# Kernel optimization log

Measured on AMD Instinct MI355X. Metric: run time of the kernel, lower is better.

The kernel has to match this reference:

```python
import jax, jax.numpy as jnp
import numpy as np

SEQ_LEN, PRED_LEN = 512, 96
D_MODEL, D_STATE, D_FF = 512, 16, 512
DT_RANK = 32  # ceil(d_model / 16)
E_LAYERS = 2
B, N = 32, 256


def _layernorm(x, g, b, eps=1e-5):
    mu = jnp.mean(x, -1, keepdims=True)
    var = jnp.mean((x - mu) ** 2, -1, keepdims=True)
    return (x - mu) * jax.lax.rsqrt(var + eps) * g + b


def _mamba(x, win, convw, convb, wx, wdt, bdt, alog, dparam, wout):
    # x: [B, T, D] with T = n_variates + 6 (inverted tokens)
    Bb, T, D = x.shape
    xz = x @ win.T                      # [B, T, 2D] (expand=1 -> d_inner = D)
    xr, z = xz[..., :D], xz[..., D:]
    # causal depthwise conv, d_conv=2: y[t] = w0*x[t-1] + w1*x[t] + b
    x_prev = jnp.pad(xr, ((0, 0), (1, 0), (0, 0)))[:, :T]
    xc = jax.nn.silu(x_prev * convw[:, 0] + xr * convw[:, 1] + convb)
    dbl = xc @ wx.T                     # [B, T, dt_rank + 2*d_state]
    dt = jax.nn.softplus(dbl[..., :DT_RANK] @ wdt.T + bdt)     # [B, T, D]
    Bm = dbl[..., DT_RANK:DT_RANK + D_STATE]                    # [B, T, S]
    Cm = dbl[..., DT_RANK + D_STATE:]                           # [B, T, S]
    A = -jnp.exp(alog)                                          # [D, S]
    dA = jnp.exp(dt[..., None] * A)                             # [B, T, D, S]
    dBx = dt[..., None] * Bm[:, :, None, :] * xc[..., None]     # [B, T, D, S]

    def step(h, inp):
        a_t, bx_t = inp
        h = a_t * h + bx_t
        return h, h

    h0 = jnp.zeros((Bb, D, D_STATE), x.dtype)
    _, hs = jax.lax.scan(step, h0, (jnp.swapaxes(dA, 0, 1), jnp.swapaxes(dBx, 0, 1)))
    y = jnp.einsum('tbds,bts->btd', hs, Cm) + dparam * xc
    y = y * jax.nn.silu(z)
    return y @ wout.T


def _forward(x_enc, x_mark_enc, emb_w, emb_b, m_win, m_convw, m_convb, m_wx, m_wdt,
             m_bdt, m_alog, m_dparam, m_wout, ln1_g, ln1_b, ff1_w, ff1_b, ff2_w,
             ff2_b, ln2_g, ln2_b, lnf_g, lnf_b, proj_w, proj_b):
    n_var = x_enc.shape[2]
    # instance norm over time (use_norm=True)
    means = jnp.mean(x_enc, 1, keepdims=True)
    xn = x_enc - means
    stdev = jnp.sqrt(jnp.var(xn, axis=1, keepdims=True) + 1e-5)
    xn = xn / stdev
    # inverted embedding: tokens = variates (+ time-feature channels), proj seq_len -> d_model
    tok = jnp.concatenate([jnp.swapaxes(xn, 1, 2), jnp.swapaxes(x_mark_enc, 1, 2)], axis=1)
    h = tok @ emb_w.T + emb_b           # [B, n_var+6, d_model]
    for l in range(E_LAYERS):
        f = _mamba(h, m_win[l, 0], m_convw[l, 0], m_convb[l, 0], m_wx[l, 0],
                   m_wdt[l, 0], m_bdt[l, 0], m_alog[l, 0], m_dparam[l, 0], m_wout[l, 0])
        r = jnp.flip(_mamba(jnp.flip(h, 1), m_win[l, 1], m_convw[l, 1], m_convb[l, 1],
                            m_wx[l, 1], m_wdt[l, 1], m_bdt[l, 1], m_alog[l, 1],
                            m_dparam[l, 1], m_wout[l, 1]), 1)
        h = _layernorm(h + f + r, ln1_g[l], ln1_b[l])
        y = jax.nn.relu(h @ ff1_w[l].T + ff1_b[l]) @ ff2_w[l].T + ff2_b[l]
        h = _layernorm(h + y, ln2_g[l], ln2_b[l])
    h = _layernorm(h, lnf_g, lnf_b)
    dec = jnp.swapaxes(h @ proj_w.T + proj_b, 1, 2)[:, :, :n_var]  # [B, pred_len, N]
    dec = dec * stdev[:, 0, :][:, None, :] + means[:, 0, :][:, None, :]
    return dec


def setup_inputs() -> dict:
    key = jax.random.key(0)
    ks = iter(jax.random.split(key, 64))

    def rn(shape, scale=0.02):
        return jax.random.normal(next(ks), shape, dtype=jnp.float32) * scale

    D, S, R, L = D_MODEL, D_STATE, DT_RANK, E_LAYERS
    return dict(
        x_enc=jax.random.normal(next(ks), (B, SEQ_LEN, N), dtype=jnp.float32),
        x_mark_enc=jax.random.uniform(next(ks), (B, SEQ_LEN, 6), dtype=jnp.float32,
                                      minval=-1.0, maxval=1.0),
        emb_w=rn((D, SEQ_LEN)), emb_b=jnp.zeros((D,), jnp.float32),
        m_win=rn((L, 2, 2 * D, D)),
        m_convw=rn((L, 2, D, 2), 0.5),
        m_convb=jnp.zeros((L, 2, D), jnp.float32),
        m_wx=rn((L, 2, R + 2 * S, D)),
        m_wdt=rn((L, 2, D, R)),
        m_bdt=jnp.full((L, 2, D), -4.6, jnp.float32),  # softplus ~= 0.01
        m_alog=jnp.broadcast_to(jnp.log(jnp.arange(1, S + 1, dtype=jnp.float32)), (L, 2, D, S)) * jnp.ones((L, 2, D, S), jnp.float32),
        m_dparam=jnp.ones((L, 2, D), jnp.float32),
        m_wout=rn((L, 2, D, D)),
        ln1_g=jnp.ones((L, D), jnp.float32), ln1_b=jnp.zeros((L, D), jnp.float32),
        ff1_w=rn((L, D_FF, D)), ff1_b=jnp.zeros((L, D_FF), jnp.float32),
        ff2_w=rn((L, D, D_FF)), ff2_b=jnp.zeros((L, D), jnp.float32),
        ln2_g=jnp.ones((L, D), jnp.float32), ln2_b=jnp.zeros((L, D), jnp.float32),
        lnf_g=jnp.ones((D,), jnp.float32), lnf_b=jnp.zeros((D,), jnp.float32),
        proj_w=rn((PRED_LEN, D)), proj_b=jnp.zeros((PRED_LEN,), jnp.float32),
    )


def reference(x_enc, x_mark_enc, emb_w, emb_b, m_win, m_convw, m_convb, m_wx, m_wdt,
              m_bdt, m_alog, m_dparam, m_wout, ln1_g, ln1_b, ff1_w, ff1_b, ff2_w,
              ff2_b, ln2_g, ln2_b, lnf_g, lnf_b, proj_w, proj_b):
    return _forward(x_enc, x_mark_enc, emb_w, emb_b, m_win, m_convw, m_convb, m_wx,
                    m_wdt, m_bdt, m_alog, m_dparam, m_wout, ln1_g, ln1_b, ff1_w,
                    ff1_b, ff2_w, ff2_b, ln2_g, ln2_b, lnf_g, lnf_b, proj_w, proj_b)
```

## Files before the change

kernel.cpp:

```cpp
#include <hip/hip_runtime.h>
#include <hip/hip_bf16.h>
#include <math.h>
#include <stddef.h>

#define BB 32
#define TT 262
#define DD 512
#define SS 16
#define RR 32
#define SEQ 512
#define NV 256
#define PRED 96
#define MROWS (BB*TT)
#define NCHK 8
#define CSZ 33

typedef __attribute__((ext_vector_type(4))) float f32x4;
typedef __attribute__((ext_vector_type(8))) short s16x8;

__device__ inline ushort f2bu(float x) {
    __hip_bfloat16 h = __float2bfloat16(x);
    ushort u; __builtin_memcpy(&u, &h, 2); return u;
}
__device__ inline float bu2f(ushort u) {
    __hip_bfloat16 h; __builtin_memcpy(&h, &u, 2);
    return __bfloat162float(h);
}

__device__ inline void gload_lds16(const void* g, void* l) {
    __builtin_amdgcn_global_load_lds(
        (const __attribute__((address_space(1))) void*)g,
        (__attribute__((address_space(3))) void*)l, 16, 0, 0);
}

__global__ __launch_bounds__(256)
void packw(const float* __restrict__ in, ushort* __restrict__ out, int total)
{
    int idx = blockIdx.x * 256 + threadIdx.x;
    if (idx >= total) return;
    out[idx] = f2bu(in[idx]);
}

__global__ __launch_bounds__(256)
void mkcomb(const float* __restrict__ wx, const float* __restrict__ wdt,
            ushort* __restrict__ comb)
{
    int n  = blockIdx.x;
    int li = blockIdx.y;
    const float* wxl = wx + (size_t)li*64*512;
    ushort* outb = comb + ((size_t)li*544 + n)*512;
    if (n < 512) {
        __shared__ float wr[32];
        if (threadIdx.x < 32)
            wr[threadIdx.x] = wdt[(size_t)li*512*32 + (size_t)n*32 + threadIdx.x];
        __syncthreads();
        for (int kk = threadIdx.x; kk < 512; kk += 256) {
            float acc = 0.f;
            #pragma unroll
            for (int r = 0; r < 32; ++r)
                acc = fmaf(wr[r], wxl[r*512 + kk], acc);
            outb[kk] = f2bu(acc);
        }
    } else {
        int s = n - 512;
        for (int kk = threadIdx.x; kk < 512; kk += 256)
            outb[kk] = f2bu(wxl[(32+s)*512 + kk]);
    }
}

__global__ __launch_bounds__(256)
void stats_kernel(const float* __restrict__ x_enc,
                  float* __restrict__ mean, float* __restrict__ stdv)
{
    int b  = blockIdx.x >> 4;
    int n0 = (blockIdx.x & 15) << 4;
    int nl = threadIdx.x & 15;
    int tg = threadIdx.x >> 4;
    int n = n0 + nl;
    const float* base = x_enc + (size_t)b*SEQ*NV + n;
    float s0 = 0.f, s1 = 0.f, q0 = 0.f, q1 = 0.f;
    #pragma unroll 8
    for (int i = 0; i < 16; ++i) {
        int t = tg + i*32;
        float v0 = base[(size_t)t*NV];
        float v1 = base[(size_t)(t+16)*NV];
        s0 += v0; q0 = fmaf(v0, v0, q0);
        s1 += v1; q1 = fmaf(v1, v1, q1);
    }
    float s = s0 + s1, q = q0 + q1;
    __shared__ float ls[16][17], lq[16][17];
    ls[tg][nl] = s; lq[tg][nl] = q;
    __syncthreads();
    if (tg < 8) { ls[tg][nl] += ls[tg+8][nl]; lq[tg][nl] += lq[tg+8][nl]; }
    __syncthreads();
    if (tg < 4) { ls[tg][nl] += ls[tg+4][nl]; lq[tg][nl] += lq[tg+4][nl]; }
    __syncthreads();
    if (tg < 2) { ls[tg][nl] += ls[tg+2][nl]; lq[tg][nl] += lq[tg+2][nl]; }
    __syncthreads();
    if (tg == 0) {
        s = ls[0][nl] + ls[1][nl];
        q = lq[0][nl] + lq[1][nl];
        float mu  = s * (1.f/SEQ);
        float var = q * (1.f/SEQ) - mu*mu;
        mean[b*NV + n] = mu;
        stdv[b*NV + n] = sqrtf(var + 1e-5f);
    }
}

__global__ __launch_bounds__(256)
void tok_kernel(const float* __restrict__ x_enc, const float* __restrict__ x_mark,
                const float* __restrict__ mean, const float* __restrict__ stdv,
                ushort* __restrict__ tokb)
{
    int b  = blockIdx.x / 40;
    int r  = blockIdx.x % 40;
    int tt = r / 5;
    int vt = r % 5;
    int t0 = tt << 6, v0 = vt << 6;
    __shared__ float tile[64][65];
    int lv = threadIdx.x & 63;
    for (int i = threadIdx.x >> 6; i < 64; i += 4) {
        int t = t0 + i, v = v0 + lv;
        float val = 0.f;
        if (v < NV) {
            val = (x_enc[((size_t)b*SEQ + t)*NV + v] - mean[b*NV + v]) / stdv[b*NV + v];
        } else if (v < TT) {
            val = x_mark[((size_t)b*SEQ + t)*6 + (v - NV)];
        }
        tile[i][lv] = val;
    }
    __syncthreads();
    for (int i = threadIdx.x >> 6; i < 64; i += 4) {
        int v = v0 + i;
        if (v < TT) {
            size_t row = (size_t)b*TT + v;
            tokb[row*512 + t0 + lv] = f2bu(tile[lv][i]);
        }
    }
}

template<int HAS_BIAS, int RELU, int WF32, int W3, int SCANEP>
__global__ __launch_bounds__(256)
void gemm3(const ushort* __restrict__ A3, int lda3,
           const ushort* __restrict__ W3p, int ldw3,
           const float* __restrict__ bias,
           float* __restrict__ C, int ldc,
           ushort* __restrict__ C3, int N_out,
           float* __restrict__ bcbuf,
           size_t aOff, size_t wOff, size_t biasOff, size_t cOff, size_t bcOff,
           int M, int Nn, int K3)
{
    const int dir = blockIdx.y;
    A3  += (size_t)dir * aOff;
    W3p += (size_t)dir * wOff;
    if (HAS_BIAS || SCANEP) bias += (size_t)dir * biasOff;
    if (WF32) C += (size_t)dir * cOff;
    if (W3 || SCANEP) C3 += (size_t)dir * cOff;
    if (SCANEP) bcbuf += (size_t)dir * bcOff;

    __shared__ ushort lds[2][192*64];
    const int tid  = threadIdx.x;
    const int lane = tid & 63;
    const int wid  = tid >> 6;
    const int wr = wid >> 1, wc = wid & 1;

    int nwg = gridDim.x;
    int q8 = nwg >> 3, r8 = nwg & 7;
    int xcd = blockIdx.x & 7;
    int idx = blockIdx.x >> 3;
    int swz = (xcd < r8 ? xcd*(q8+1) : r8*(q8+1) + (xcd-r8)*q8) + idx;
    int ntile = (Nn + 63) >> 6;
    const int m0 = (swz / ntile) * 128;
    const int n0 = (swz % ntile) * 64;

    const int l8 = lane >> 3;
    const int sl = lane & 7;
    const int ssl = sl ^ l8;

    int arow[4], wrow[2];
    #pragma unroll
    for (int qq = 0; qq < 4; ++qq) {
        int r = (wid*4 + qq)*8 + l8;
        int ar = m0 + r; if (ar > M-1) ar = M-1;
        arow[qq] = ar;
    }
    #pragma unroll
    for (int qq = 0; qq < 2; ++qq) {
        int r = (wid*2 + qq)*8 + l8;
        int wrr = n0 + r; if (wrr > Nn-1) wrr = Nn-1;
        wrow[qq] = wrr;
    }

    f32x4 acc[4][2];
    #pragma unroll
    for (int i = 0; i < 4; ++i)
        #pragma unroll
        for (int j = 0; j < 2; ++j) acc[i][j] = (f32x4){0.f,0.f,0.f,0.f};

    const int nk = K3 >> 6;
    const int rl = lane & 15;
    const int kq = lane >> 4;

    auto stage = [&](int buf_, int kt_) {
        #pragma unroll
        for (int qq = 0; qq < 4; ++qq) {
            int c = wid*4 + qq;
            gload_lds16(A3 + (size_t)arow[qq]*lda3 + kt_*64 + ssl*8,
                        (void*)&lds[buf_][c*512]);
        }
        #pragma unroll
        for (int qq = 0; qq < 2; ++qq) {
            int c = wid*2 + qq;
            gload_lds16(W3p + (size_t)wrow[qq]*ldw3 + kt_*64 + ssl*8,
                        (void*)&lds[buf_][8192 + c*512]);
        }
    };

    stage(0, 0);
    __syncthreads();

    for (int kt = 0; kt < nk; ++kt) {
        int cur = kt & 1;
        if (kt + 1 < nk) stage(cur ^ 1, kt + 1);
        #pragma unroll
        for (int kk = 0; kk < 2; ++kk) {
            s16x8 av[4], wv[2];
            #pragma unroll
            for (int mi = 0; mi < 4; ++mi) {
                int row = wr*64 + mi*16 + rl;
                int ck = (kk*4 + kq) ^ (row & 7);
                av[mi] = *(const s16x8*)&lds[cur][row*64 + (ck<<3)];
            }
            #pragma unroll
            for (int ni = 0; ni < 2; ++ni) {
                int row = wc*32 + ni*16 + rl;
                int ck = (kk*4 + kq) ^ (row & 7);
                wv[ni] = *(const s16x8*)&lds[cur][8192 + row*64 + (ck<<3)];
            }
            #pragma unroll
            for (int mi = 0; mi < 4; ++mi)
                #pragma unroll
                for (int ni = 0; ni < 2; ++ni)
                    acc[mi][ni] = __builtin_amdgcn_mfma_f32_16x16x32_bf16(
                        av[mi], wv[ni], acc[mi][ni], 0, 0, 0);
        }
        __syncthreads();
    }

    #pragma unroll
    for (int ni = 0; ni < 2; ++ni) {
        int n = n0 + wc*32 + ni*16 + rl;
        if (n >= Nn) continue;
        float bv = (HAS_BIAS && !SCANEP) ? bias[n] : 0.f;
        #pragma unroll
        for (int mi = 0; mi < 4; ++mi) {
            #pragma unroll
            for (int j = 0; j < 4; ++j) {
                int m = m0 + wr*64 + mi*16 + kq*4 + j;
                if (m >= M) continue;
                float v = acc[mi][ni][j];
                if (SCANEP) {
                    if (n < 512) {
                        v += bias[n];
                        v = fmaxf(v, 0.f) + log1pf(__expf(-fabsf(v)));
                        C3[(size_t)m*ldc + n] = f2bu(v);
                    } else {
                        bcbuf[(size_t)m*N_out + (n - 512)] = v;
                    }
                } else {
                    if (HAS_BIAS) v += bv;
                    if (RELU) v = fmaxf(v, 0.f);
                    if (WF32) C[(size_t)m*ldc + n] = v;
                    if (W3)   C3[(size_t)m*N_out + n] = f2bu(v);
                }
            }
        }
    }
}

__global__ __launch_bounds__(256)
void conv2(ushort* __restrict__ xzb, const float* __restrict__ cwB,
           const float* __restrict__ cbB, float* __restrict__ xc,
           ushort* __restrict__ xcb)
{
    int gid = blockIdx.x * 256 + threadIdx.x;
    int d = gid & 511;
    int r = gid >> 9;
    int dir = (r >= MROWS) ? 1 : 0;
    int bt = r - dir*MROWS;
    int t = bt % TT;
    const float* cw = cwB + dir*DD*2;
    const float* cb = cbB + dir*DD;
    size_t base = (size_t)bt*2048 + (size_t)dir*1024;
    float cur = bu2f(xzb[base + d]);
    int tn = dir ? t + 1 : t - 1;
    float prev = 0.f;
    if (tn >= 0 && tn < TT)
        prev = bu2f(xzb[base + (dir ? 2048 : -2048) + d]);
    float v = prev*cw[d*2] + cur*cw[d*2+1] + cb[d];
    float sv = v / (1.f + __expf(-v));
    size_t o = (size_t)bt*1024 + dir*512 + d;
    xc[o] = sv;
    xcb[o] = f2bu(sv);
    float z = bu2f(xzb[base + 512 + d]);
    xzb[base + 512 + d] = f2bu(z / (1.f + __expf(-z)));
}

__global__ __launch_bounds__(256)
void scan_p1(const ushort* __restrict__ sp_g, const float* __restrict__ xc_g,
             const float* __restrict__ bc_g, const float* __restrict__ alog,
             float* __restrict__ hs, float* __restrict__ ps)
{
    int dir = blockIdx.z;
    int rev = dir;
    sp_g += dir*512; xc_g += dir*512; bc_g += dir*32;
    alog += (size_t)dir*DD*SS;
    size_t doff = (size_t)dir*(NCHK-1)*65536*4;
    hs += doff; ps += doff;

    int sblk = blockIdx.x;
    int c    = blockIdx.y;
    int b  = sblk >> 3;
    int d0 = (sblk & 7) << 6;
    int tid = threadIdx.x;
    int sg = tid & 3;
    int dl = tid >> 2;
    int d  = d0 + dl;

    float Ac[4];
    #pragma unroll
    for (int j = 0; j < 4; ++j)
        Ac[j] = -__expf(alog[d*SS + sg*4 + j]);
    float h0=0.f,h1=0.f,h2=0.f,h3=0.f;
    float p0=1.f,p1=1.f,p2=1.f,p3=1.f;
    size_t bbase = (size_t)b*TT;
    int t0 = c*CSZ;
    #pragma unroll 3
    for (int i = 0; i < CSZ; ++i) {
        int t = t0 + i;
        size_t p = bbase + (rev ? TT-1-t : t);
        float spv = bu2f(sp_g[p*1024 + d]);
        float xcv = xc_g[p*1024 + d];
        float4 Bv = *(const float4*)(bc_g + p*64 + sg*4);
        float dtxc = spv*xcv;
        float e0 = __expf(spv*Ac[0]);
        float e1 = __expf(spv*Ac[1]);
        float e2 = __expf(spv*Ac[2]);
        float e3 = __expf(spv*Ac[3]);
        h0 = fmaf(e0,h0,dtxc*Bv.x); p0 *= e0;
        h1 = fmaf(e1,h1,dtxc*Bv.y); p1 *= e1;
        h2 = fmaf(e2,h2,dtxc*Bv.z); p2 *= e2;
        h3 = fmaf(e3,h3,dtxc*Bv.w); p3 *= e3;
    }
    size_t o = ((size_t)c*256 + sblk)*256 + tid;
    float4 hv; hv.x=h0; hv.y=h1; hv.z=h2; hv.w=h3;
    float4 pv; pv.x=p0; pv.y=p1; pv.z=p2; pv.w=p3;
    ((float4*)hs)[o] = hv;
    ((float4*)ps)[o] = pv;
}

__global__ __launch_bounds__(256)
void scan_comb(const float* __restrict__ hs, const float* __restrict__ ps,
               float* __restrict__ hin)
{
    int dir = blockIdx.y;
    size_t doff = (size_t)dir*(NCHK-1)*65536;
    size_t gid = (size_t)blockIdx.x*256 + threadIdx.x;
    float4 h = {0.f,0.f,0.f,0.f};
    for (int c = 0; c < NCHK-1; ++c) {
        size_t o = doff + (size_t)c*65536 + gid;
        float4 hl = ((const float4*)hs)[o];
        float4 pv = ((const float4*)ps)[o];
        h.x = fmaf(pv.x, h.x, hl.x);
        h.y = fmaf(pv.y, h.y, hl.y);
        h.z = fmaf(pv.z, h.z, hl.z);
        h.w = fmaf(pv.w, h.w, hl.w);
        ((float4*)hin)[o] = h;
    }
}

__global__ __launch_bounds__(256)
void scan_p2(const ushort* __restrict__ sp_g, const float* __restrict__ xc_g,
             const ushort* __restrict__ xz_u, const float* __restrict__ bc_g,
             const float* __restrict__ alog, const float* __restrict__ dparam,
             const float* __restrict__ hin, ushort* __restrict__ yb)
{
    int dir = blockIdx.z;
    int rev = dir;
    sp_g += dir*512; xc_g += dir*512; bc_g += dir*32; xz_u += dir*1024;
    alog += (size_t)dir*DD*SS; dparam += (size_t)dir*DD;
    hin += (size_t)dir*(NCHK-1)*65536*4;
    yb  += (size_t)dir*(size_t)MROWS*512;

    int sblk = blockIdx.x;
    int c    = blockIdx.y;
    int b  = sblk >> 3;
    int d0 = (sblk & 7) << 6;
    int tid = threadIdx.x;
    int sg = tid & 3;
    int dl = tid >> 2;
    int d  = d0 + dl;

    float Ac[4];
    #pragma unroll
    for (int j = 0; j < 4; ++j)
        Ac[j] = -__expf(alog[d*SS + sg*4 + j]);
    float dp = dparam[d];
    float h0=0.f,h1=0.f,h2=0.f,h3=0.f;
    if (c > 0) {
        float4 hv = ((const float4*)hin)[((size_t)(c-1)*256 + sblk)*256 + tid];
        h0=hv.x; h1=hv.y; h2=hv.z; h3=hv.w;
    }
    size_t bbase = (size_t)b*TT;
    int t0 = c*CSZ;
    #pragma unroll 3
    for (int i = 0; i < CSZ; ++i) {
        int t = t0 + i;
        int tc = t < TT ? t : TT-1;
        size_t p = bbase + (rev ? TT-1-tc : tc);
        float spv = bu2f(sp_g[p*1024 + d]);
        float xcv = xc_g[p*1024 + d];
        float zsv = bu2f(xz_u[p*2048 + 512 + d]);
        float4 Bv = *(const float4*)(bc_g + p*64 + sg*4);
        float4 Cv = *(const float4*)(bc_g + p*64 + 16 + sg*4);
        float dtxc = spv*xcv;
        float e0 = __expf(spv*Ac[0]);
        float e1 = __expf(spv*Ac[1]);
        float e2 = __expf(spv*Ac[2]);
        float e3 = __expf(spv*Ac[3]);
        h0 = fmaf(e0,h0,dtxc*Bv.x);
        h1 = fmaf(e1,h1,dtxc*Bv.y);
        h2 = fmaf(e2,h2,dtxc*Bv.z);
        h3 = fmaf(e3,h3,dtxc*Bv.w);
        float dot = h0*Cv.x + h1*Cv.y + h2*Cv.z + h3*Cv.w;
        dot += __shfl_xor(dot, 1);
        dot += __shfl_xor(dot, 2);
        if (sg == 0 && t < TT) {
            int tg = rev ? TT-1-t : t;
            float yv = (dot + dp*xcv) * zsv;
            yb[(bbase + tg)*512 + d] = f2bu(yv);
        }
    }
}

__global__ __launch_bounds__(64)
void ln_kernel(float* __restrict__ dst, const float* __restrict__ a,
               const float* __restrict__ b, const float* __restrict__ c,
               const float* __restrict__ g, const float* __restrict__ beta,
               ushort* __restrict__ outb)
{
    int row = blockIdx.x;
    int lane = threadIdx.x;
    size_t base = (size_t)row * DD;
    float x[8];
    #pragma unroll
    for (int j = 0; j < 2; ++j) {
        int e4 = j*64 + lane;
        float4 v = *(const float4*)(a + base + (size_t)e4*4);
        if (b) { float4 t = *(const float4*)(b + base + (size_t)e4*4); v.x+=t.x; v.y+=t.y; v.z+=t.z; v.w+=t.w; }
        if (c) { float4 t = *(const float4*)(c + base + (size_t)e4*4); v.x+=t.x; v.y+=t.y; v.z+=t.z; v.w+=t.w; }
        x[j*4+0]=v.x; x[j*4+1]=v.y; x[j*4+2]=v.z; x[j*4+3]=v.w;
    }
    float s = 0.f;
    #pragma unroll
    for (int i = 0; i < 8; ++i) s += x[i];
    #pragma unroll
    for (int m = 1; m < 64; m <<= 1) s += __shfl_xor(s, m);
    float mu = s * (1.f/DD);
    float vs = 0.f;
    #pragma unroll
    for (int i = 0; i < 8; ++i) { float dd = x[i]-mu; vs += dd*dd; }
    #pragma unroll
    for (int m = 1; m < 64; m <<= 1) vs += __shfl_xor(vs, m);
    float r = rsqrtf(vs*(1.f/DD) + 1e-5f);
    #pragma unroll
    for (int j = 0; j < 2; ++j) {
        int e4 = j*64 + lane;
        float4 gv = *(const float4*)(g    + (size_t)e4*4);
        float4 bv = *(const float4*)(beta + (size_t)e4*4);
        float4 o;
        o.x = (x[j*4+0]-mu)*r*gv.x + bv.x;
        o.y = (x[j*4+1]-mu)*r*gv.y + bv.y;
        o.z = (x[j*4+2]-mu)*r*gv.z + bv.z;
        o.w = (x[j*4+3]-mu)*r*gv.w + bv.w;
        *(float4*)(dst + base + (size_t)e4*4) = o;
        if (outb) {
            ushort* ob = outb + (size_t)row*512;
            ob[e4*4+0] = f2bu(o.x);
            ob[e4*4+1] = f2bu(o.y);
            ob[e4*4+2] = f2bu(o.z);
            ob[e4*4+3] = f2bu(o.w);
        }
    }
}

__global__ __launch_bounds__(256)
void proj_fin(const float* __restrict__ projtmp, const float* __restrict__ mean,
              const float* __restrict__ stdv, float* __restrict__ out)
{
    int b  = blockIdx.x >> 2;
    int n0 = (blockIdx.x & 3) << 6;
    __shared__ float tile[64][97];
    for (int i = threadIdx.x; i < 64*96; i += 256) {
        int rj = i / 96, cp = i % 96;
        tile[rj][cp] = projtmp[((size_t)b*TT + n0 + rj)*96 + cp];
    }
    __syncthreads();
    int nl = threadIdx.x & 63;
    int pg = threadIdx.x >> 6;
    int n = n0 + nl;
    float sd = stdv[b*NV + n];
    float mu = mean[b*NV + n];
    #pragma unroll
    for (int i = 0; i < 24; ++i) {
        int p = pg*24 + i;
        out[((size_t)b*PRED + p)*NV + n] = tile[nl][p]*sd + mu;
    }
}

extern "C" void kernel_launch(void* const* d_in, const int* in_sizes, int n_in,
                              void* d_out, int out_size, void* d_ws, size_t ws_size,
                              hipStream_t stream)
{
    (void)in_sizes; (void)n_in; (void)out_size; (void)ws_size;
    const float* x_enc   = (const float*)d_in[0];
    const float* x_mark  = (const float*)d_in[1];
    const float* emb_w   = (const float*)d_in[2];
    const float* emb_b   = (const float*)d_in[3];
    const float* m_win   = (const float*)d_in[4];
    const float* m_convw = (const float*)d_in[5];
    const float* m_convb = (const float*)d_in[6];
    const float* m_wx    = (const float*)d_in[7];
    const float* m_wdt   = (const float*)d_in[8];
    const float* m_bdt   = (const float*)d_in[9];
    const float* m_alog  = (const float*)d_in[10];
    const float* m_dpar  = (const float*)d_in[11];
    const float* m_wout  = (const float*)d_in[12];
    const float* ln1_g   = (const float*)d_in[13];
    const float* ln1_b   = (const float*)d_in[14];
    const float* ff1_w   = (const float*)d_in[15];
    const float* ff1_b   = (const float*)d_in[16];
    const float* ff2_w   = (const float*)d_in[17];
    const float* ff2_b   = (const float*)d_in[18];
    const float* ln2_g   = (const float*)d_in[19];
    const float* ln2_b   = (const float*)d_in[20];
    const float* lnf_g   = (const float*)d_in[21];
    const float* lnf_b   = (const float*)d_in[22];
    const float* proj_w  = (const float*)d_in[23];
    const float* proj_b  = (const float*)d_in[24];
    float* out = (float*)d_out;

    float* ws = (float*)d_ws;
    const size_t NBT = (size_t)MROWS;
    size_t off = 0;
    float* mean = ws + off; off += 8192;
    float* stdv = ws + off; off += 8192;
    ushort* w_emb  = (ushort*)(ws + off); off += 131072;
    ushort* w_win  = (ushort*)(ws + off); off += 1048576;
    ushort* w_wout = (ushort*)(ws + off); off += 524288;
    ushort* w_ff1  = (ushort*)(ws + off); off += 262144;
    ushort* w_ff2  = (ushort*)(ws + off); off += 262144;
    ushort* w_comb = (ushort*)(ws + off); off += 557056;
    ushort* w_proj = (ushort*)(ws + off); off += 24576;
    ushort* pool = (ushort*)(ws + off); off += NBT*768;
    ushort* tokb = pool;
    ushort* xcb  = pool;
    ushort* yb   = pool;
    float* h   = ws + off; off += NBT*512;
    ushort* hb = (ushort*)(ws + off); off += NBT*256;
    ushort* xzb = (ushort*)(ws + off); off += NBT*1024;
    ushort* fftb = xzb;
    ushort* spb = (ushort*)(ws + off); off += NBT*512;
    float* xcf = ws + off; off += NBT*1024;
    float* xs  = ws + off; off += NBT*512;
    float* bc2 = ws + off; off += NBT*64;
    float* fbuf = ws + off; off += NBT*512;
    float* rbuf = ws + off; off += NBT*512;
    float* hs  = ws + off; off += (size_t)2*(NCHK-1)*65536*4;
    float* psb = ws + off; off += (size_t)2*(NCHK-1)*65536*4;
    float* hin = ws + off; off += (size_t)2*(NCHK-1)*65536*4;
    float* projtmp = ws + off; off += NBT*96;
    (void)rbuf;

    packw<<<dim3((512*512+255)/256),  256, 0, stream>>>(emb_w, w_emb, 512*512);
    packw<<<dim3((4096*512+255)/256), 256, 0, stream>>>(m_win, w_win, 4096*512);
    packw<<<dim3((2048*512+255)/256), 256, 0, stream>>>(m_wout, w_wout, 2048*512);
    packw<<<dim3((1024*512+255)/256), 256, 0, stream>>>(ff1_w, w_ff1, 1024*512);
    packw<<<dim3((1024*512+255)/256), 256, 0, stream>>>(ff2_w, w_ff2, 1024*512);
    packw<<<dim3((96*512+255)/256),   256, 0, stream>>>(proj_w, w_proj, 96*512);
    mkcomb<<<dim3(544,4), 256, 0, stream>>>(m_wx, m_wdt, w_comb);

    stats_kernel<<<dim3(BB*16), 256, 0, stream>>>(x_enc, mean, stdv);
    tok_kernel<<<dim3(BB*40), 256, 0, stream>>>(x_enc, x_mark, mean, stdv, tokb);

    gemm3<1,0,1,1,0><<<dim3(66*8), 256, 0, stream>>>(tokb, 512, w_emb, 512,
        emb_b, h, DD, hb, 512, nullptr, 0,0,0,0,0, MROWS, 512, 512);

    for (int l = 0; l < 2; ++l) {
        gemm3<0,0,0,1,0><<<dim3(66*32), 256, 0, stream>>>(hb, 512,
            w_win + (size_t)l*2048*512, 512, nullptr,
            nullptr, 0, xzb, 2048, nullptr, 0,0,0,0,0, MROWS, 2048, 512);
        conv2<<<dim3((2*MROWS*DD)/256), 256, 0, stream>>>(xzb,
            m_convw + (size_t)l*2*DD*2, m_convb + (size_t)l*2*DD, xcf, xcb);
        gemm3<0,0,0,0,1><<<dim3(66*9, 2), 256, 0, stream>>>(
            xcb, 1024, w_comb + (size_t)l*2*544*512, 512,
            m_bdt + (size_t)l*2*DD, nullptr, 1024, spb, 64, bc2,
            512, (size_t)544*512, 512,
            512, 32, MROWS, 544, 512);
        const float* al = m_alog + (size_t)l*2*DD*SS;
        const float* dpp = m_dpar + (size_t)l*2*DD;
        scan_p1<<<dim3(256, NCHK-1, 2), 256, 0, stream>>>(spb, xcf, bc2, al,
            hs, psb);
        scan_comb<<<dim3(256, 2), 256, 0, stream>>>(hs, psb, hin);
        scan_p2<<<dim3(256, NCHK, 2), 256, 0, stream>>>(spb, xcf, xzb, bc2,
            al, dpp, hin, yb);
        gemm3<0,0,1,0,0><<<dim3(66*8, 2), 256, 0, stream>>>(yb, 512,
            w_wout + (size_t)l*2*512*512, 512, nullptr,
            fbuf, DD, nullptr, 0, nullptr,
            NBT*512, (size_t)512*512, 0,
            NBT*512, 0, MROWS, 512, 512);
        ln_kernel<<<dim3(MROWS), 64, 0, stream>>>(h, h, fbuf, rbuf,
            ln1_g + l*DD, ln1_b + l*DD, hb);
        gemm3<1,1,0,1,0><<<dim3(66*8), 256, 0, stream>>>(hb, 512,
            w_ff1 + (size_t)l*512*512, 512, ff1_b + l*DD,
            nullptr, 0, fftb, 512, nullptr, 0,0,0,0,0, MROWS, 512, 512);
        gemm3<1,0,1,0,0><<<dim3(66*8), 256, 0, stream>>>(fftb, 512,
            w_ff2 + (size_t)l*512*512, 512, ff2_b + l*DD,
            xs, DD, nullptr, 0, nullptr, 0,0,0,0,0, MROWS, 512, 512);
        ln_kernel<<<dim3(MROWS), 64, 0, stream>>>(h, h, xs, nullptr,
            ln2_g + l*DD, ln2_b + l*DD, hb);
    }
    ln_kernel<<<dim3(MROWS), 64, 0, stream>>>(fbuf, h, nullptr, nullptr,
                                              lnf_g, lnf_b, hb);
    gemm3<1,0,1,0,0><<<dim3(66*2), 256, 0, stream>>>(hb, 512, w_proj, 512,
        proj_b, projtmp, 96, nullptr, 0, nullptr, 0,0,0,0,0, MROWS, 96, 512);
    proj_fin<<<dim3(BB*4), 256, 0, stream>>>(projtmp, mean, stdv, out);
}
```

Before: 659.4 us.

## Replace chunked three-pass selective scan with single sequential full-length scan kernel

Replaces the chunked scan (partial pass, combine pass, second pass over 8 time chunks) with one kernel that walks all 262 timesteps per thread, using pointer-stride addressing and software prefetch of the next timestep's inputs. This removes two kernel launches, the intermediate state buffers and the redundant recompute of the exponentials in the first pass. The cost is that the launch shrinks from thousands of blocks to 512, so parallelism drops and each thread carries a long serial dependency chain, which could leave the GPU underutilised.

New measurement: 691.3 us. 4.8% more time.

```diff
diff --git a/kernel.cpp b/kernel.cpp
--- a/kernel.cpp
+++ b/kernel.cpp
@@ -12,8 +12,6 @@
 #define NV 256
 #define PRED 96
 #define MROWS (BB*TT)
-#define NCHK 8
-#define CSZ 33
 
 typedef __attribute__((ext_vector_type(4))) float f32x4;
 typedef __attribute__((ext_vector_type(8))) short s16x8;
@@ -307,19 +305,18 @@
 }
 
 __global__ __launch_bounds__(256)
-void scan_p1(const ushort* __restrict__ sp_g, const float* __restrict__ xc_g,
-             const float* __restrict__ bc_g, const float* __restrict__ alog,
-             float* __restrict__ hs, float* __restrict__ ps)
-{
-    int dir = blockIdx.z;
+void scan_full(const ushort* __restrict__ sp_g, const float* __restrict__ xc_g,
+               const ushort* __restrict__ xz_u, const float* __restrict__ bc_g,
+               const float* __restrict__ alog, const float* __restrict__ dparam,
+               ushort* __restrict__ yb)
+{
+    int dir = blockIdx.y;
     int rev = dir;
-    sp_g += dir*512; xc_g += dir*512; bc_g += dir*32;
-    alog += (size_t)dir*DD*SS;
-    size_t doff = (size_t)dir*(NCHK-1)*65536*4;
-    hs += doff; ps += doff;
+    sp_g += dir*512; xc_g += dir*512; bc_g += dir*32; xz_u += dir*1024;
+    alog += (size_t)dir*DD*SS; dparam += (size_t)dir*DD;
+    yb  += (size_t)dir*(size_t)MROWS*512;
 
     int sblk = blockIdx.x;
-    int c    = blockIdx.y;
     int b  = sblk >> 3;
     int d0 = (sblk & 7) << 6;
     int tid = threadIdx.x;
@@ -331,115 +328,58 @@
     #pragma unroll
     for (int j = 0; j < 4; ++j)
         Ac[j] = -__expf(alog[d*SS + sg*4 + j]);
-    float h0=0.f,h1=0.f,h2=0.f,h3=0.f;
-    float p0=1.f,p1=1.f,p2=1.f,p3=1.f;
+    float dp = dparam[d];
+
     size_t bbase = (size_t)b*TT;
-    int t0 = c*CSZ;
-    #pragma unroll 3
-    for (int i = 0; i < CSZ; ++i) {
-        int t = t0 + i;
-        size_t p = bbase + (rev ? TT-1-t : t);
-        float spv = bu2f(sp_g[p*1024 + d]);
-        float xcv = xc_g[p*1024 + d];
-        float4 Bv = *(const float4*)(bc_g + p*64 + sg*4);
-        float dtxc = spv*xcv;
-        float e0 = __expf(spv*Ac[0]);
-        float e1 = __expf(spv*Ac[1]);
-        float e2 = __expf(spv*Ac[2]);
-        float e3 = __expf(spv*Ac[3]);
-        h0 = fmaf(e0,h0,dtxc*Bv.x); p0 *= e0;
-        h1 = fmaf(e1,h1,dtxc*Bv.y); p1 *= e1;
-        h2 = fmaf(e2,h2,dtxc*Bv.z); p2 *= e2;
-        h3 = fmaf(e3,h3,dtxc*Bv.w); p3 *= e3;
-    }
-    size_t o = ((size_t)c*256 + sblk)*256 + tid;
-    float4 hv; hv.x=h0; hv.y=h1; hv.z=h2; hv.w=h3;
-    float4 pv; pv.x=p0; pv.y=p1; pv.z=p2; pv.w=p3;
-    ((float4*)hs)[o] = hv;
-    ((float4*)ps)[o] = pv;
-}
-
-__global__ __launch_bounds__(256)
-void scan_comb(const float* __restrict__ hs, const float* __restrict__ ps,
-               float* __restrict__ hin)
-{
-    int dir = blockIdx.y;
-    size_t doff = (size_t)dir*(NCHK-1)*65536;
-    size_t gid = (size_t)blockIdx.x*256 + threadIdx.x;
-    float4 h = {0.f,0.f,0.f,0.f};
-    for (int c = 0; c < NCHK-1; ++c) {
-        size_t o = doff + (size_t)c*65536 + gid;
-        float4 hl = ((const float4*)hs)[o];
-        float4 pv = ((const float4*)ps)[o];
-        h.x = fmaf(pv.x, h.x, hl.x);
-        h.y = fmaf(pv.y, h.y, hl.y);
-        h.z = fmaf(pv.z, h.z, hl.z);
-        h.w = fmaf(pv.w, h.w, hl.w);
-        ((float4*)hin)[o] = h;
-    }
-}
-
-__global__ __launch_bounds__(256)
-void scan_p2(const ushort* __restrict__ sp_g, const float* __restrict__ xc_g,
-             const ushort* __restrict__ xz_u, const float* __restrict__ bc_g,
-             const float* __restrict__ alog, const float* __restrict__ dparam,
-             const float* __restrict__ hin, ushort* __restrict__ yb)
-{
-    int dir = blockIdx.z;
-    int rev = dir;
-    sp_g += dir*512; xc_g += dir*512; bc_g += dir*32; xz_u += dir*1024;
-    alog += (size_t)dir*DD*SS; dparam += (size_t)dir*DD;
-    hin += (size_t)dir*(NCHK-1)*65536*4;
-    yb  += (size_t)dir*(size_t)MROWS*512;
-
-    int sblk = blockIdx.x;
-    int c    = blockIdx.y;
-    int b  = sblk >> 3;
-    int d0 = (sblk & 7) << 6;
-    int tid = threadIdx.x;
-    int sg = tid & 3;
-    int dl = tid >> 2;
-    int d  = d0 + dl;
-
-    float Ac[4];
-    #pragma unroll
-    for (int j = 0; j < 4; ++j)
-        Ac[j] = -__expf(alog[d*SS + sg*4 + j]);
-    float dp = dparam[d];
-    float h0=0.f,h1=0.f,h2=0.f,h3=0.f;
-    if (c > 0) {
-        float4 hv = ((const float4*)hin)[((size_t)(c-1)*256 + sblk)*256 + tid];
-        h0=hv.x; h1=hv.y; h2=hv.z; h3=hv.w;
-    }
-    size_t bbase = (size_t)b*TT;
-    int t0 = c*CSZ;
-    #pragma unroll 3
-    for (int i = 0; i < CSZ; ++i) {
-        int t = t0 + i;
-        int tc = t < TT ? t : TT-1;
-        size_t p = bbase + (rev ? TT-1-tc : tc);
-        float spv = bu2f(sp_g[p*1024 + d]);
-        float xcv = xc_g[p*1024 + d];
-        float zsv = bu2f(xz_u[p*2048 + 512 + d]);
-        float4 Bv = *(const float4*)(bc_g + p*64 + sg*4);
-        float4 Cv = *(const float4*)(bc_g + p*64 + 16 + sg*4);
-        float dtxc = spv*xcv;
-        float e0 = __expf(spv*Ac[0]);
-        float e1 = __expf(spv*Ac[1]);
-        float e2 = __expf(spv*Ac[2]);
-        float e3 = __expf(spv*Ac[3]);
-        h0 = fmaf(e0,h0,dtxc*Bv.x);
-        h1 = fmaf(e1,h1,dtxc*Bv.y);
-        h2 = fmaf(e2,h2,dtxc*Bv.z);
-        h3 = fmaf(e3,h3,dtxc*Bv.w);
-        float dot = h0*Cv.x + h1*Cv.y + h2*Cv.z + h3*Cv.w;
+    size_t pstart = bbase + (rev ? TT-1 : 0);
+    ptrdiff_t stp = rev ? -1 : 1;
+    const ushort* spp = sp_g + pstart*1024 + d;
+    const float*  xcp = xc_g + pstart*1024 + d;
+    const ushort* zpp = xz_u + pstart*2048 + 512 + d;
+    const float*  bcp = bc_g + pstart*64 + sg*4;
+    ushort* ybp = yb + pstart*512 + d;
+    const ptrdiff_t sp_s = stp*1024;
+    const ptrdiff_t z_s  = stp*2048;
+    const ptrdiff_t bc_s = stp*64;
+    const ptrdiff_t yb_s = stp*512;
+
+    float h0=0.f, h1=0.f, h2=0.f, h3=0.f;
+
+    float sp_c = bu2f(*spp);
+    float xc_c = *xcp;
+    float z_c  = bu2f(*zpp);
+    float4 B_c = *(const float4*)bcp;
+    float4 C_c = *(const float4*)(bcp + 16);
+
+    for (int t = 0; t < TT; ++t) {
+        float sp_n = 0.f, xc_n = 0.f, z_n = 0.f;
+        float4 B_n = {0,0,0,0}, C_n = {0,0,0,0};
+        if (t + 1 < TT) {
+            spp += sp_s; xcp += sp_s; zpp += z_s; bcp += bc_s;
+            sp_n = bu2f(*spp);
+            xc_n = *xcp;
+            z_n  = bu2f(*zpp);
+            B_n  = *(const float4*)bcp;
+            C_n  = *(const float4*)(bcp + 16);
+        }
+        float dtxc = sp_c * xc_c;
+        float e0 = __expf(sp_c*Ac[0]);
+        float e1 = __expf(sp_c*Ac[1]);
+        float e2 = __expf(sp_c*Ac[2]);
+        float e3 = __expf(sp_c*Ac[3]);
+        h0 = fmaf(e0, h0, dtxc*B_c.x);
+        h1 = fmaf(e1, h1, dtxc*B_c.y);
+        h2 = fmaf(e2, h2, dtxc*B_c.z);
+        h3 = fmaf(e3, h3, dtxc*B_c.w);
+        float dot = h0*C_c.x + h1*C_c.y + h2*C_c.z + h3*C_c.w;
         dot += __shfl_xor(dot, 1);
         dot += __shfl_xor(dot, 2);
-        if (sg == 0 && t < TT) {
-            int tg = rev ? TT-1-t : t;
-            float yv = (dot + dp*xcv) * zsv;
-            yb[(bbase + tg)*512 + d] = f2bu(yv);
-        }
+        if (sg == 0) {
+            float yv = (dot + dp*xc_c) * z_c;
+            *ybp = f2bu(yv);
+        }
+        ybp += yb_s;
+        sp_c = sp_n; xc_c = xc_n; z_c = z_n; B_c = B_n; C_c = C_n;
     }
 }
 
@@ -576,9 +516,6 @@
     float* bc2 = ws + off; off += NBT*64;
     float* fbuf = ws + off; off += NBT*512;
     float* rbuf = ws + off; off += NBT*512;
-    float* hs  = ws + off; off += (size_t)2*(NCHK-1)*65536*4;
-    float* psb = ws + off; off += (size_t)2*(NCHK-1)*65536*4;
-    float* hin = ws + off; off += (size_t)2*(NCHK-1)*65536*4;
     float* projtmp = ws + off; off += NBT*96;
     (void)rbuf;
 
@@ -609,11 +546,8 @@
             512, 32, MROWS, 544, 512);
         const float* al = m_alog + (size_t)l*2*DD*SS;
         const float* dpp = m_dpar + (size_t)l*2*DD;
-        scan_p1<<<dim3(256, NCHK-1, 2), 256, 0, stream>>>(spb, xcf, bc2, al,
-            hs, psb);
-        scan_comb<<<dim3(256, 2), 256, 0, stream>>>(hs, psb, hin);
-        scan_p2<<<dim3(256, NCHK, 2), 256, 0, stream>>>(spb, xcf, xzb, bc2,
-            al, dpp, hin, yb);
+        scan_full<<<dim3(256, 2), 256, 0, stream>>>(spb, xcf, xzb, bc2,
+            al, dpp, yb);
         gemm3<0,0,1,0,0><<<dim3(66*8, 2), 256, 0, stream>>>(yb, 512,
             w_wout + (size_t)l*2*512*512, 512, nullptr,
             fbuf, DD, nullptr, 0, nullptr,
```
